# Kernel tuning notes

Measured on AMD Instinct MI355X. Metric: run time of the kernel, lower is better.

## Reference

```python
import jax, jax.numpy as jnp
import numpy as np

B, T, D = 128, 256, 1024

def setup_inputs() -> dict:
    key = jax.random.key(0)
    ks = jax.random.split(key, 7)
    s = 1.0 / np.sqrt(D)
    return {
        "inputs": jax.random.normal(ks[0], (B, T, D), dtype=jnp.float32),
        "Wk": jax.random.uniform(ks[1], (D, D), jnp.float32, -s, s),
        "bk": jax.random.uniform(ks[2], (D,), jnp.float32, -s, s),
        "Wq": jax.random.uniform(ks[3], (D, D), jnp.float32, -s, s),
        "bq": jax.random.uniform(ks[4], (D,), jnp.float32, -s, s),
        "Wv": jax.random.uniform(ks[5], (D, D), jnp.float32, -s, s),
        "bv": jax.random.uniform(ks[6], (D,), jnp.float32, -s, s),
    }

def reference(inputs, Wk, bk, Wq, bq, Wv, bv):
    # torch.nn.Linear: y = x @ W.T + b
    keys = inputs @ Wk.T + bk        # [B, T, D]
    queries = inputs @ Wq.T + bq     # [B, T, D]
    values = inputs @ Wv.T + bv      # [B, T, D]
    scale = 1.0 / jnp.sqrt(jnp.float32(inputs.shape[-1]))
    scores = jnp.einsum('btd,bsd->bts', queries, keys) * scale  # [B, T, T]
    t = inputs.shape[1]
    causal = jnp.tril(jnp.ones((t, t), dtype=bool))
    scores = jnp.where(causal, scores, -jnp.inf)
    probs = jax.nn.softmax(scores, axis=-1)
    return jnp.einsum('bts,bsd->btd', probs, values)
```

## Files before the change

### kernel.cpp

```cpp
#include <hip/hip_runtime.h>
#include <hip/hip_bf16.h>


typedef __attribute__((ext_vector_type(4))) float f32x4;
typedef __attribute__((ext_vector_type(8))) short s16x8;
typedef unsigned short u16;

__device__ inline u16 f2bf(float f) {
    union { __hip_bfloat16 h; u16 u; } c;
    c.h = __float2bfloat16(f);
    return c.u;
}

__device__ __forceinline__ void stage16(const void* g, void* l) {
    __builtin_amdgcn_global_load_lds((const __attribute__((address_space(1))) void*)g,
                                     (__attribute__((address_space(3))) void*)l, 16, 0, 0);
}

#define MFMA(a_, b_, c_) (c_) = __builtin_amdgcn_mfma_f32_16x16x32_bf16((a_), (b_), (c_), 0, 0, 0)

__global__ __launch_bounds__(256) void cvt_f32_bf16(const float* __restrict__ in,
                                                    u16* __restrict__ out, int n4) {
    int stride = gridDim.x * blockDim.x;
    for (int i = blockIdx.x * blockDim.x + threadIdx.x; i < n4; i += stride) {
        float4 v = reinterpret_cast<const float4*>(in)[i];
        ushort4 o = make_ushort4(f2bf(v.x), f2bf(v.y), f2bf(v.z), f2bf(v.w));
        reinterpret_cast<ushort4*>(out)[i] = o;
    }
}

__global__ __launch_bounds__(512, 2) void qkv256(const u16* __restrict__ X, const u16* __restrict__ W3,
                                                 const float* __restrict__ biasK,
                                                 const float* __restrict__ biasQ,
                                                 const float* __restrict__ biasV,
                                                 u16* __restrict__ Kb, u16* __restrict__ Qb,
                                                 u16* __restrict__ Vt) {
    extern __shared__ char lds[];

    const int bid = blockIdx.x;
    const int swz = (bid & 7) * 192 + (bid >> 3);
    const int mt = swz / 12, nt2 = swz % 12;
    const int nmat = nt2 >> 2, ncol = nt2 & 3;
    const u16* Asrc = X + (size_t)mt * 256 * 1024;
    const u16* Bsrc = W3 + (size_t)nmat * 1048576 + (size_t)ncol * 256 * 1024;

    const int tid  = threadIdx.x;
    const int lane = tid & 63, w = tid >> 6;
    const int wr = w >> 2, wc = w & 3;
    const int l15 = lane & 15, l16 = lane >> 4;

    const int lds_ro = l15 * 64 + ((l16 ^ ((l15 >> 1) & 3)) << 4);
    const int aoff = wr * 128 * 64 + lds_ro;
    const int boff = 16384 + wc * 64 * 64 + lds_ro;

    const int isB = w >> 2;
    const u16* dsrc = isB ? Bsrc : Asrc;
    const int drow  = (w & 3) * 64 + (lane >> 2);
    const int dslot = ((lane & 3) ^ ((lane >> 3) & 3)) * 8;
    const u16* dptr0 = dsrc + (size_t)drow * 1024 + dslot;
    const int dlds = isB * 16384 + (w & 3) * 4096;

#define STAGE(u_) do {                                                            \
        char* bb_ = lds + (((u_) & 3) * 32768) + dlds;                            \
        const u16* gp_ = dptr0 + (size_t)(u_) * 32;                               \
        stage16(gp_,             bb_);                                            \
        stage16(gp_ + 16 * 1024, bb_ + 1024);                                     \
        stage16(gp_ + 32 * 1024, bb_ + 2048);                                     \
        stage16(gp_ + 48 * 1024, bb_ + 3072);                                     \
    } while (0)

#define RDA(d_, bp_, fm_) d_[fm_] = *(const s16x8*)((bp_) + aoff + (fm_) * 1024)
#define RDB(d_, bp_, fn_) d_[fn_] = *(const s16x8*)((bp_) + boff + (fn_) * 1024)

#define MM4(fm_, a_, b_) do {                                                     \
        MFMA(a_[fm_], b_[0], acc[fm_][0]);                                        \
        MFMA(a_[fm_], b_[1], acc[fm_][1]);                                        \
        MFMA(a_[fm_], b_[2], acc[fm_][2]);                                        \
        MFMA(a_[fm_], b_[3], acc[fm_][3]);                                        \
    } while (0)

#define STEP(u_, AR_, BR_, AM_, BM_) do {                                         \
        if ((u_) + 2 <= 31) STAGE((u_) + 2);                                      \
        const char* bp_ = lds + (((u_) & 3) * 32768);                             \
        RDA(AR_, bp_, 0); RDA(AR_, bp_, 1); RDA(AR_, bp_, 2);                     \
        MM4(0, AM_, BM_); MM4(1, AM_, BM_);                                       \
        RDA(AR_, bp_, 3); RDA(AR_, bp_, 4); RDA(AR_, bp_, 5);                     \
        MM4(2, AM_, BM_); MM4(3, AM_, BM_);                                       \
        RDA(AR_, bp_, 6); RDA(AR_, bp_, 7); RDB(BR_, bp_, 0);                     \
        MM4(4, AM_, BM_); MM4(5, AM_, BM_);                                       \
        RDB(BR_, bp_, 1); RDB(BR_, bp_, 2); RDB(BR_, bp_, 3);                     \
        MM4(6, AM_, BM_); MM4(7, AM_, BM_);                                       \
        if ((u_) <= 29) asm volatile("s_waitcnt vmcnt(4)" ::: "memory");          \
        else            asm volatile("s_waitcnt vmcnt(0)" ::: "memory");          \
        __builtin_amdgcn_s_barrier();                                             \
    } while (0)

    f32x4 acc[8][4] = {};
    s16x8 a0[8], b0[4], a1[8], b1[4];

    STAGE(0); STAGE(1); STAGE(2);
    asm volatile("s_waitcnt vmcnt(4)" ::: "memory");
    __builtin_amdgcn_s_barrier();
    {
        const char* bp_ = lds;
        RDA(a0, bp_, 0); RDA(a0, bp_, 1); RDA(a0, bp_, 2); RDA(a0, bp_, 3);
        RDA(a0, bp_, 4); RDA(a0, bp_, 5); RDA(a0, bp_, 6); RDA(a0, bp_, 7);
        RDB(b0, bp_, 0); RDB(b0, bp_, 1); RDB(b0, bp_, 2); RDB(b0, bp_, 3);
    }

    for (int tt = 0; tt < 15; ++tt) {
        STEP(2 * tt + 1, a1, b1, a0, b0);
        STEP(2 * tt + 2, a0, b0, a1, b1);
    }
    STEP(31, a1, b1, a0, b0);
    MM4(0, a1, b1); MM4(1, a1, b1); MM4(2, a1, b1); MM4(3, a1, b1);
    MM4(4, a1, b1); MM4(5, a1, b1); MM4(6, a1, b1); MM4(7, a1, b1);

#undef STAGE
#undef RDA
#undef RDB
#undef MM4
#undef STEP

    const float* bias = (nmat == 0) ? biasK : (nmat == 1) ? biasQ : biasV;
    u16* outKQ = (nmat == 0) ? Kb : Qb;
    const int colbase = ncol * 256 + wc * 64;
#pragma unroll
    for (int FM = 0; FM < 8; ++FM) {
#pragma unroll
        for (int fn = 0; fn < 4; ++fn) {
            const int col = colbase + fn * 16 + l15;
            const float bvv = bias[col];
            const int rbase = mt * 256 + wr * 128 + FM * 16 + (l16 << 2);
#pragma unroll
            for (int j = 0; j < 4; ++j) {
                const int row = rbase + j;
                const u16 hb = f2bf(acc[FM][fn][j] + bvv);
                if (nmat == 2) {
                    const int b = row >> 8, tt2 = row & 255;
                    Vt[(size_t)b * 262144 + (size_t)col * 256 + tt2] = hb;
                } else {
                    outKQ[(size_t)row * 1024 + col] = hb;
                }
            }
        }
    }
}

__device__ inline void gemm_mainloop(const u16* __restrict__ Ap, const u16* __restrict__ Bp,
                                     int lda, int ldb, int kLen,
                                     u16* As, u16* Bs, f32x4 (&acc)[4][4]) {
    const int tid  = threadIdx.x;
    const int lane = tid & 63;
    const int wr   = (tid >> 7) & 1;
    const int wc   = (tid >> 6) & 1;
    const int sr   = tid >> 3;
    const int sc   = (tid & 7) << 3;

    for (int k0 = 0; k0 < kLen; k0 += 64) {
#pragma unroll
        for (int it = 0; it < 4; ++it) {
            int r = it * 32 + sr;
            *reinterpret_cast<s16x8*>(&As[r * 64 + sc]) =
                *reinterpret_cast<const s16x8*>(&Ap[(size_t)r * lda + k0 + sc]);
            *reinterpret_cast<s16x8*>(&Bs[r * 64 + sc]) =
                *reinterpret_cast<const s16x8*>(&Bp[(size_t)r * ldb + k0 + sc]);
        }
        __syncthreads();
#pragma unroll
        for (int kk = 0; kk < 64; kk += 32) {
            const int kcol = kk + (lane >> 4) * 8;
            s16x8 a[4], bfr[4];
#pragma unroll
            for (int m = 0; m < 4; ++m)
                a[m] = *reinterpret_cast<const s16x8*>(&As[(wr * 64 + m * 16 + (lane & 15)) * 64 + kcol]);
#pragma unroll
            for (int n = 0; n < 4; ++n)
                bfr[n] = *reinterpret_cast<const s16x8*>(&Bs[(wc * 64 + n * 16 + (lane & 15)) * 64 + kcol]);
#pragma unroll
            for (int m = 0; m < 4; ++m)
#pragma unroll
                for (int n = 0; n < 4; ++n)
                    acc[m][n] = __builtin_amdgcn_mfma_f32_16x16x32_bf16(a[m], bfr[n], acc[m][n], 0, 0, 0);
        }
        __syncthreads();
    }
}

__global__ __launch_bounds__(256) void scores_gemm(const u16* __restrict__ Qb,
                                                   const u16* __restrict__ Kb,
                                                   float* __restrict__ S) {
    __shared__ u16 As[128 * 64];
    __shared__ u16 Bs[128 * 64];
    const int bid = blockIdx.x;
    const int b   = bid / 3;
    const int rem = bid % 3;
    const int ti  = (rem == 0) ? 0 : 1;
    const int si  = (rem == 2) ? 1 : 0;
    const u16* Ap = Qb + ((size_t)b * 256 + (size_t)ti * 128) * 1024;
    const u16* Bp = Kb + ((size_t)b * 256 + (size_t)si * 128) * 1024;

    f32x4 acc[4][4] = {};
    gemm_mainloop(Ap, Bp, 1024, 1024, 1024, As, Bs, acc);

    const int tid  = threadIdx.x;
    const int lane = tid & 63;
    const int wr   = (tid >> 7) & 1;
    const int wc   = (tid >> 6) & 1;
    const int r0 = (lane >> 4) << 2;
    const int c0 = lane & 15;
    const float scale = 0.03125f;
#pragma unroll
    for (int m = 0; m < 4; ++m) {
#pragma unroll
        for (int n = 0; n < 4; ++n) {
            const int s = si * 128 + wc * 64 + n * 16 + c0;
#pragma unroll
            for (int j = 0; j < 4; ++j) {
                const int t = ti * 128 + wr * 64 + m * 16 + r0 + j;
                float v = acc[m][n][j] * scale;
                if (s > t) v = -__builtin_inff();
                S[(size_t)b * 65536 + (size_t)t * 256 + s] = v;
            }
        }
    }
}

__global__ __launch_bounds__(256) void softmax_p(const float* __restrict__ S, u16* __restrict__ P) {
    const int row  = blockIdx.x * 4 + (threadIdx.x >> 6);
    const int lane = threadIdx.x & 63;
    const int b = row >> 8, t = row & 255;
    const float* Sp = S + (size_t)b * 65536 + (size_t)t * 256;
    const int s0 = lane * 4;
    float4 v = reinterpret_cast<const float4*>(Sp)[lane];
    const float NEG = -__builtin_inff();
    float x0 = (s0 + 0 <= t) ? v.x : NEG;
    float x1 = (s0 + 1 <= t) ? v.y : NEG;
    float x2 = (s0 + 2 <= t) ? v.z : NEG;
    float x3 = (s0 + 3 <= t) ? v.w : NEG;
    float mx = fmaxf(fmaxf(x0, x1), fmaxf(x2, x3));
#pragma unroll
    for (int off = 1; off < 64; off <<= 1) mx = fmaxf(mx, __shfl_xor(mx, off, 64));
    float e0 = (s0 + 0 <= t) ? __expf(x0 - mx) : 0.f;
    float e1 = (s0 + 1 <= t) ? __expf(x1 - mx) : 0.f;
    float e2 = (s0 + 2 <= t) ? __expf(x2 - mx) : 0.f;
    float e3 = (s0 + 3 <= t) ? __expf(x3 - mx) : 0.f;
    float sum = e0 + e1 + e2 + e3;
#pragma unroll
    for (int off = 1; off < 64; off <<= 1) sum += __shfl_xor(sum, off, 64);
    const float inv = 1.0f / sum;
    ushort4 o = make_ushort4(f2bf(e0 * inv), f2bf(e1 * inv), f2bf(e2 * inv), f2bf(e3 * inv));
    reinterpret_cast<ushort4*>(P + (size_t)row * 256)[lane] = o;
}

__global__ __launch_bounds__(256) void pv_gemm(const u16* __restrict__ P, const u16* __restrict__ Vt,
                                               float* __restrict__ O) {
    __shared__ u16 As[128 * 64];
    __shared__ u16 Bs[128 * 64];
    const int bid = blockIdx.x;
    const int b   = bid >> 4;
    const int r   = bid & 15;
    const int mt  = r >> 3;
    const int ntl = r & 7;
    const u16* Ap = P + (size_t)b * 65536 + (size_t)mt * 128 * 256;
    const u16* Bp = Vt + (size_t)b * 262144 + (size_t)ntl * 128 * 256;
    const int kmax = (mt + 1) * 128;

    f32x4 acc[4][4] = {};
    gemm_mainloop(Ap, Bp, 256, 256, kmax, As, Bs, acc);

    const int tid  = threadIdx.x;
    const int lane = tid & 63;
    const int wr   = (tid >> 7) & 1;
    const int wc   = (tid >> 6) & 1;
    const int r0 = (lane >> 4) << 2;
    const int c0 = lane & 15;
#pragma unroll
    for (int m = 0; m < 4; ++m) {
#pragma unroll
        for (int n = 0; n < 4; ++n) {
            const int d = ntl * 128 + wc * 64 + n * 16 + c0;
#pragma unroll
            for (int j = 0; j < 4; ++j) {
                const int t = mt * 128 + wr * 64 + m * 16 + r0 + j;
                O[((size_t)b * 256 + t) * 1024 + d] = acc[m][n][j];
            }
        }
    }
}

extern "C" void kernel_launch(void* const* d_in, const int* in_sizes, int n_in,
                              void* d_out, int out_size, void* d_ws, size_t ws_size,
                              hipStream_t stream) {
    (void)in_sizes; (void)n_in; (void)out_size; (void)ws_size;
    const float* x  = (const float*)d_in[0];
    const float* Wk = (const float*)d_in[1];
    const float* bk = (const float*)d_in[2];
    const float* Wq = (const float*)d_in[3];
    const float* bq = (const float*)d_in[4];
    const float* Wv = (const float*)d_in[5];
    const float* bv = (const float*)d_in[6];
    float* out = (float*)d_out;
    char* ws = (char*)d_ws;

    u16*   xb = (u16*)(ws + 0);
    u16*   Wb = (u16*)(ws + 67108864);
    u16*   Kb = (u16*)(ws + 73400320);
    u16*   Qb = (u16*)(ws + 140509184);
    u16*   Vt = (u16*)(ws + 207618048);
    float* S  = (float*)(ws + 0);
    u16*   P  = (u16*)(ws + 33554432);

    cvt_f32_bf16<<<2048, 256, 0, stream>>>(x, xb, 33554432 / 4);
    cvt_f32_bf16<<<512, 256, 0, stream>>>(Wk, Wb, 1048576 / 4);
    cvt_f32_bf16<<<512, 256, 0, stream>>>(Wq, Wb + 1048576, 1048576 / 4);
    cvt_f32_bf16<<<512, 256, 0, stream>>>(Wv, Wb + 2097152, 1048576 / 4);
    qkv256<<<1536, 512, 131072, stream>>>(xb, Wb, bk, bq, bv, Kb, Qb, Vt);
    scores_gemm<<<384, 256, 0, stream>>>(Qb, Kb, S);
    softmax_p<<<8192, 256, 0, stream>>>(S, P);
    pv_gemm<<<2048, 256, 0, stream>>>(P, Vt, out);
}
```

Baseline: 405.6 us.

## Fuse causal softmax into scores GEMM epilogue and pad LDS rows

Replaces the separate scores GEMM, which wrote fp32 scores to global memory, and the softmax kernel with one kernel. Each 512-thread block computes a full 128-row by up-to-256-column score tile, applies the mask, reduces max and sum across waves through shared memory, and writes bf16 probabilities directly. This removes the fp32 score round trip and one launch. LDS row stride is also padded from 64 to 72 elements in the GEMM mainloops to reduce bank conflicts. In exchange only 256 blocks are launched, with uneven work between the two row halves, which may leave compute units underused.

```diff
diff --git a/kernel.cpp b/kernel.cpp
--- a/kernel.cpp
+++ b/kernel.cpp
@@ -147,6 +147,135 @@
     }
 }
 
+__global__ __launch_bounds__(512, 2) void scores_sm2(const u16* __restrict__ Qb,
+                                                     const u16* __restrict__ Kb,
+                                                     u16* __restrict__ P) {
+    __shared__ u16 As[128 * 72];
+    __shared__ u16 Bs[256 * 72];
+    __shared__ float redM[4][128];
+    __shared__ float redS[4][128];
+
+    const int bid = blockIdx.x;
+    const int b = bid >> 1, ti = bid & 1;
+    const int nN = 2 << ti;
+    const int nBrow = 128 << ti;
+    const u16* Ap = Qb + ((size_t)b * 256 + (size_t)ti * 128) * 1024;
+    const u16* Bp = Kb + (size_t)b * 256 * 1024;
+
+    const int tid  = threadIdx.x;
+    const int lane = tid & 63;
+    const int w    = tid >> 6;
+    const int wr   = w >> 2, wc = w & 3;
+    const int l15  = lane & 15, l16 = lane >> 4;
+    const int sr   = tid >> 3;
+    const int sc   = (tid & 7) << 3;
+
+    f32x4 acc[4][4] = {};
+
+    for (int k0 = 0; k0 < 1024; k0 += 64) {
+#pragma unroll
+        for (int it = 0; it < 2; ++it) {
+            const int r = it * 64 + sr;
+            *reinterpret_cast<s16x8*>(&As[r * 72 + sc]) =
+                *reinterpret_cast<const s16x8*>(&Ap[(size_t)r * 1024 + k0 + sc]);
+        }
+#pragma unroll
+        for (int it = 0; it < 4; ++it) {
+            if (it * 64 < nBrow) {
+                const int r = it * 64 + sr;
+                *reinterpret_cast<s16x8*>(&Bs[r * 72 + sc]) =
+                    *reinterpret_cast<const s16x8*>(&Bp[(size_t)r * 1024 + k0 + sc]);
+            }
+        }
+        __syncthreads();
+#pragma unroll
+        for (int kk = 0; kk < 64; kk += 32) {
+            const int kcol = kk + l16 * 8;
+            s16x8 a[4], bb[4];
+#pragma unroll
+            for (int m = 0; m < 4; ++m)
+                a[m] = *reinterpret_cast<const s16x8*>(&As[(wr * 64 + m * 16 + l15) * 72 + kcol]);
+#pragma unroll
+            for (int n = 0; n < 4; ++n)
+                if (n < nN)
+                    bb[n] = *reinterpret_cast<const s16x8*>(&Bs[(wc * 16 * nN + n * 16 + l15) * 72 + kcol]);
+#pragma unroll
+            for (int m = 0; m < 4; ++m)
+#pragma unroll
+                for (int n = 0; n < 4; ++n)
+                    if (n < nN)
+                        MFMA(a[m], bb[n], acc[m][n]);
+        }
+        __syncthreads();
+    }
+
+    const int r0 = l16 << 2;
+    const float scale = 0.03125f;
+    const float NEG = -__builtin_inff();
+
+#pragma unroll
+    for (int m = 0; m < 4; ++m) {
+#pragma unroll
+        for (int j = 0; j < 4; ++j) {
+            const int rr = wr * 64 + m * 16 + r0 + j;
+            const int t_ = ti * 128 + rr;
+            float mx = NEG;
+#pragma unroll
+            for (int n = 0; n < 4; ++n)
+                if (n < nN) {
+                    const int s_ = wc * 16 * nN + n * 16 + l15;
+                    float v = acc[m][n][j] * scale;
+                    v = (s_ <= t_) ? v : NEG;
+                    acc[m][n][j] = v;
+                    mx = fmaxf(mx, v);
+                }
+#pragma unroll
+            for (int off = 1; off < 16; off <<= 1) mx = fmaxf(mx, __shfl_xor(mx, off, 64));
+            if (l15 == 0) redM[wc][rr] = mx;
+        }
+    }
+    __syncthreads();
+
+#pragma unroll
+    for (int m = 0; m < 4; ++m) {
+#pragma unroll
+        for (int j = 0; j < 4; ++j) {
+            const int rr = wr * 64 + m * 16 + r0 + j;
+            const float MX = fmaxf(fmaxf(redM[0][rr], redM[1][rr]),
+                                   fmaxf(redM[2][rr], redM[3][rr]));
+            float s = 0.f;
+#pragma unroll
+            for (int n = 0; n < 4; ++n)
+                if (n < nN) {
+                    float e = __expf(acc[m][n][j] - MX);
+                    acc[m][n][j] = e;
+                    s += e;
+                }
+#pragma unroll
+            for (int off = 1; off < 16; off <<= 1) s += __shfl_xor(s, off, 64);
+            if (l15 == 0) redS[wc][rr] = s;
+        }
+    }
+    __syncthreads();
+
+#pragma unroll
+    for (int m = 0; m < 4; ++m) {
+#pragma unroll
+        for (int j = 0; j < 4; ++j) {
+            const int rr = wr * 64 + m * 16 + r0 + j;
+            const int t_ = ti * 128 + rr;
+            const float inv = 1.0f / (redS[0][rr] + redS[1][rr] + redS[2][rr] + redS[3][rr]);
+            u16* Pr = P + (size_t)b * 65536 + (size_t)t_ * 256;
+#pragma unroll
+            for (int n = 0; n < 4; ++n)
+                if (n < nN) {
+                    const int s_ = wc * 16 * nN + n * 16 + l15;
+                    Pr[s_] = f2bf(acc[m][n][j] * inv);
+                }
+        }
+    }
+}
+
 __device__ inline void gemm_mainloop(const u16* __restrict__ Ap, const u16* __restrict__ Bp,
                                      int lda, int ldb, int kLen,
                                      u16* As, u16* Bs, f32x4 (&acc)[4][4]) {
@@ -161,9 +290,9 @@
 #pragma unroll
         for (int it = 0; it < 4; ++it) {
             int r = it * 32 + sr;
-            *reinterpret_cast<s16x8*>(&As[r * 64 + sc]) =
+            *reinterpret_cast<s16x8*>(&As[r * 72 + sc]) =
                 *reinterpret_cast<const s16x8*>(&Ap[(size_t)r * lda + k0 + sc]);
-            *reinterpret_cast<s16x8*>(&Bs[r * 64 + sc]) =
+            *reinterpret_cast<s16x8*>(&Bs[r * 72 + sc]) =
                 *reinterpret_cast<const s16x8*>(&Bp[(size_t)r * ldb + k0 + sc]);
         }
         __syncthreads();
@@ -173,10 +302,10 @@
             s16x8 a[4], bfr[4];
 #pragma unroll
             for (int m = 0; m < 4; ++m)
-                a[m] = *reinterpret_cast<const s16x8*>(&As[(wr * 64 + m * 16 + (lane & 15)) * 64 + kcol]);
-#pragma unroll
-            for (int n = 0; n < 4; ++n)
-                bfr[n] = *reinterpret_cast<const s16x8*>(&Bs[(wc * 64 + n * 16 + (lane & 15)) * 64 + kcol]);
+                a[m] = *reinterpret_cast<const s16x8*>(&As[(wr * 64 + m * 16 + (lane & 15)) * 72 + kcol]);
+#pragma unroll
+            for (int n = 0; n < 4; ++n)
+                bfr[n] = *reinterpret_cast<const s16x8*>(&Bs[(wc * 64 + n * 16 + (lane & 15)) * 72 + kcol]);
 #pragma unroll
             for (int m = 0; m < 4; ++m)
 #pragma unroll
@@ -187,76 +316,10 @@
     }
 }
 
-__global__ __launch_bounds__(256) void scores_gemm(const u16* __restrict__ Qb,
-                                                   const u16* __restrict__ Kb,
-                                                   float* __restrict__ S) {
-    __shared__ u16 As[128 * 64];
-    __shared__ u16 Bs[128 * 64];
-    const int bid = blockIdx.x;
-    const int b   = bid / 3;
-    const int rem = bid % 3;
-    const int ti  = (rem == 0) ? 0 : 1;
-    const int si  = (rem == 2) ? 1 : 0;
-    const u16* Ap = Qb + ((size_t)b * 256 + (size_t)ti * 128) * 1024;
-    const u16* Bp = Kb + ((size_t)b * 256 + (size_t)si * 128) * 1024;
-
-    f32x4 acc[4][4] = {};
-    gemm_mainloop(Ap, Bp, 1024, 1024, 1024, As, Bs, acc);
-
-    const int tid  = threadIdx.x;
-    const int lane = tid & 63;
-    const int wr   = (tid >> 7) & 1;
-    const int wc   = (tid >> 6) & 1;
-    const int r0 = (lane >> 4) << 2;
-    const int c0 = lane & 15;
-    const float scale = 0.03125f;
-#pragma unroll
-    for (int m = 0; m < 4; ++m) {
-#pragma unroll
-        for (int n = 0; n < 4; ++n) {
-            const int s = si * 128 + wc * 64 + n * 16 + c0;
-#pragma unroll
-            for (int j = 0; j < 4; ++j) {
-                const int t = ti * 128 + wr * 64 + m * 16 + r0 + j;
-                float v = acc[m][n][j] * scale;
-                if (s > t) v = -__builtin_inff();
-                S[(size_t)b * 65536 + (size_t)t * 256 + s] = v;
-            }
-        }
-    }
-}
-
-__global__ __launch_bounds__(256) void softmax_p(const float* __restrict__ S, u16* __restrict__ P) {
-    const int row  = blockIdx.x * 4 + (threadIdx.x >> 6);
-    const int lane = threadIdx.x & 63;
-    const int b = row >> 8, t = row & 255;
-    const float* Sp = S + (size_t)b * 65536 + (size_t)t * 256;
-    const int s0 = lane * 4;
-    float4 v = reinterpret_cast<const float4*>(Sp)[lane];
-    const float NEG = -__builtin_inff();
-    float x0 = (s0 + 0 <= t) ? v.x : NEG;
-    float x1 = (s0 + 1 <= t) ? v.y : NEG;
-    float x2 = (s0 + 2 <= t) ? v.z : NEG;
-    float x3 = (s0 + 3 <= t) ? v.w : NEG;
-    float mx = fmaxf(fmaxf(x0, x1), fmaxf(x2, x3));
-#pragma unroll
-    for (int off = 1; off < 64; off <<= 1) mx = fmaxf(mx, __shfl_xor(mx, off, 64));
-    float e0 = (s0 + 0 <= t) ? __expf(x0 - mx) : 0.f;
-    float e1 = (s0 + 1 <= t) ? __expf(x1 - mx) : 0.f;
-    float e2 = (s0 + 2 <= t) ? __expf(x2 - mx) : 0.f;
-    float e3 = (s0 + 3 <= t) ? __expf(x3 - mx) : 0.f;
-    float sum = e0 + e1 + e2 + e3;
-#pragma unroll
-    for (int off = 1; off < 64; off <<= 1) sum += __shfl_xor(sum, off, 64);
-    const float inv = 1.0f / sum;
-    ushort4 o = make_ushort4(f2bf(e0 * inv), f2bf(e1 * inv), f2bf(e2 * inv), f2bf(e3 * inv));
-    reinterpret_cast<ushort4*>(P + (size_t)row * 256)[lane] = o;
-}
-
 __global__ __launch_bounds__(256) void pv_gemm(const u16* __restrict__ P, const u16* __restrict__ Vt,
                                                float* __restrict__ O) {
-    __shared__ u16 As[128 * 64];
-    __shared__ u16 Bs[128 * 64];
+    __shared__ u16 As[128 * 72];
+    __shared__ u16 Bs[128 * 72];
     const int bid = blockIdx.x;
     const int b   = bid >> 4;
     const int r   = bid & 15;
@@ -308,7 +371,6 @@
     u16*   Kb = (u16*)(ws + 73400320);
     u16*   Qb = (u16*)(ws + 140509184);
     u16*   Vt = (u16*)(ws + 207618048);
-    float* S  = (float*)(ws + 0);
     u16*   P  = (u16*)(ws + 33554432);
 
     cvt_f32_bf16<<<2048, 256, 0, stream>>>(x, xb, 33554432 / 4);
@@ -316,7 +378,6 @@
     cvt_f32_bf16<<<512, 256, 0, stream>>>(Wq, Wb + 1048576, 1048576 / 4);
     cvt_f32_bf16<<<512, 256, 0, stream>>>(Wv, Wb + 2097152, 1048576 / 4);
     qkv256<<<1536, 512, 131072, stream>>>(xb, Wb, bk, bq, bv, Kb, Qb, Vt);
-    scores_gemm<<<384, 256, 0, stream>>>(Qb, Kb, S);
-    softmax_p<<<8192, 256, 0, stream>>>(S, P);
+    scores_sm2<<<256, 512, 0, stream>>>(Qb, Kb, P);
     pv_gemm<<<2048, 256, 0, stream>>>(P, Vt, out);
 }
```

Measured after the change: 412.7 us. About the same (+1.8%).
